# Kernel optimization log

Measured on AMD Instinct MI355X. Metric: run time of the kernel, lower is better.

Reference implementation:

```python
import jax, jax.numpy as jnp
import numpy as np

B = 131072      # batch of states
N_ACT = 40      # output_dim (Tetris action space)


def setup_inputs() -> dict:
    key = jax.random.key(0)
    ks = jax.random.split(key, 9)
    # state vector: 11 real-valued board features, 1 hold-piece id in [0,4),
    # 3 next-piece ids in [1,8) (0 is treated as invalid by the original code)
    keep = jax.random.normal(ks[0], (B, 11), dtype=jnp.float32)
    hold = jax.random.randint(ks[1], (B, 1), 0, 4).astype(jnp.float32)
    nxt = jax.random.randint(ks[2], (B, 3), 1, 8).astype(jnp.float32)
    x = jnp.concatenate([keep, hold, nxt], axis=1)  # [B, 15]
    W1 = jax.random.normal(ks[3], (36, 128), dtype=jnp.float32) * 0.1
    b1 = jnp.zeros((128,), dtype=jnp.float32)
    W2 = jax.random.normal(ks[4], (128, 512), dtype=jnp.float32) * 0.05
    b2 = jnp.zeros((512,), dtype=jnp.float32)
    W4 = jax.random.normal(ks[5], (512, N_ACT), dtype=jnp.float32) * 0.05
    b4 = jnp.zeros((N_ACT,), dtype=jnp.float32)
    return {"x": x, "W1": W1, "b1": b1, "W2": W2, "b2": b2, "W4": W4, "b4": b4}


def reference(x, W1, b1, W2, b2, W4, b4):
    B_, _ = x.shape
    keep = x[:, :11]                                      # [B, 11]
    # vectorized replacement of the per-sample .item() one-hot loop
    hold_idx = jax.lax.stop_gradient(jnp.clip(x[:, 11].astype(jnp.int32), 0, 3))
    nxt_idx = jax.lax.stop_gradient(jnp.clip(x[:, 12:15].astype(jnp.int32) - 1, 0, 6))
    hold_oh = jax.nn.one_hot(hold_idx, 4, dtype=x.dtype)  # [B, 4]
    nxt_oh = jax.nn.one_hot(nxt_idx, 7, dtype=x.dtype).reshape(B_, 21)  # [B, 21]
    inp = jnp.concatenate([keep, hold_oh, nxt_oh], axis=1)  # [B, 36]
    h = jax.nn.relu(inp @ W1 + b1)   # [B, 128]
    h = jax.nn.relu(h @ W2 + b2)     # [B, 512]
    return h @ W4 + b4               # [B, N_ACT]
```

## Files before the change

kernel.cpp:

```cpp
#include <hip/hip_runtime.h>


typedef short bf16x8 __attribute__((ext_vector_type(8)));
typedef float f32x4 __attribute__((ext_vector_type(4)));
typedef unsigned int u32;

#define NW1F 8192
#define NW2F 65536
#define NW4F 24576
#define PACK_TOTAL (NW1F + NW2F + NW4F)
#define PACK_THREADS (PACK_TOTAL / 8)

__device__ __forceinline__ unsigned short f2bf(float f) {
  union { float f; unsigned u; } a; a.f = f;
  unsigned r = a.u + 0x7fffu + ((a.u >> 16) & 1u);
  return (unsigned short)(r >> 16);
}
__device__ __forceinline__ u32 cvtpk(float lo, float hi) {
  u32 r;
  asm("v_cvt_pk_bf16_f32 %0, %1, %2" : "=v"(r) : "v"(lo), "v"(hi));
  return r;
}

__global__ void pack_weights(const float* __restrict__ W1,
                             const float* __restrict__ W2,
                             const float* __restrict__ W4,
                             unsigned short* __restrict__ wf) {
  int t = blockIdx.x * 256 + threadIdx.x;
  if (t >= PACK_THREADS) return;
  int fid = t >> 6, lane = t & 63;
  int l16 = lane & 15, quad = lane >> 4;
  float vals[8];
  if (fid < 16) {
    int mt = fid >> 1, ks = fid & 1;
    int m = mt * 16 + l16, k0 = ks * 32 + quad * 8;
#pragma unroll
    for (int j = 0; j < 8; ++j) { int k = k0 + j; vals[j] = (k < 36) ? W1[k * 128 + m] : 0.f; }
  } else if (fid < 144) {
    int f = fid - 16, mt = f >> 2, ks = f & 3;
    int m = mt * 16 + l16, k0 = ks * 32 + quad * 8;
#pragma unroll
    for (int j = 0; j < 8; ++j) vals[j] = W2[(k0 + j) * 512 + m];
  } else {
    int f = fid - 144, mt = f >> 4, ks = f & 15;
    int m = mt * 16 + l16, k0 = ks * 32 + quad * 8;
#pragma unroll
    for (int j = 0; j < 8; ++j) vals[j] = (m < 40) ? W4[(k0 + j) * 40 + m] : 0.f;
  }
  u32 p[4];
#pragma unroll
  for (int j = 0; j < 4; ++j) p[j] = cvtpk(vals[2 * j], vals[2 * j + 1]);
  *(bf16x8*)(wf + (size_t)t * 8) = *(bf16x8*)p;
}

__global__ __launch_bounds__(256, 2) void dqn_fused(
    const float* __restrict__ x,
    const unsigned short* __restrict__ wf,
    const float* __restrict__ b1,
    const float* __restrict__ b2,
    const float* __restrict__ b4,
    float* __restrict__ out) {
  __shared__ __align__(16) unsigned short sBuf[4 * 64 * 72];

  const int tid  = threadIdx.x;
  const int lane = tid & 63;
  const int wave = tid >> 6;
  const int quad = lane >> 4;
  const int l16  = lane & 15;
  const int row0 = blockIdx.x << 8;
  const int lr0  = wave * 64;
  unsigned short* su = sBuf + wave * (64 * 72);

  {
    const float* xr = x + (size_t)(row0 + lr0 + lane) * 15;
    unsigned short* dst = su + lane * 72;
    bf16x8 z = {0, 0, 0, 0, 0, 0, 0, 0};
#pragma unroll
    for (int c = 8; c < 64; c += 8) *(bf16x8*)(dst + c) = z;
    u32 p[4];
#pragma unroll
    for (int i = 0; i < 4; ++i) p[i] = cvtpk(xr[2 * i], xr[2 * i + 1]);
    *(bf16x8*)dst = *(bf16x8*)p;
    *(u32*)(dst + 8) = cvtpk(xr[8], xr[9]);
    dst[10] = f2bf(xr[10]);
    int hold = (int)xr[11]; hold = hold < 0 ? 0 : (hold > 3 ? 3 : hold);
    dst[11 + hold] = 0x3F80;
#pragma unroll
    for (int t = 0; t < 3; ++t) {
      int nx = (int)xr[12 + t] - 1; nx = nx < 0 ? 0 : (nx > 6 ? 6 : nx);
      dst[15 + t * 7 + nx] = 0x3F80;
    }
  }

  const f32x4 vzero = {0.f, 0.f, 0.f, 0.f};

  bf16x8 ib[4][2];
#pragma unroll
  for (int rg = 0; rg < 4; ++rg)
#pragma unroll
    for (int ks = 0; ks < 2; ++ks)
      ib[rg][ks] = *(const bf16x8*)(su + (rg * 16 + l16) * 72 + ks * 32 + quad * 8);

  bf16x8 af1[4][4];
#pragma unroll
  for (int half = 0; half < 2; ++half) {
    f32x4 acc1[4][4];
#pragma unroll
    for (int mtl = 0; mtl < 4; ++mtl)
#pragma unroll
      for (int rg = 0; rg < 4; ++rg) acc1[mtl][rg] = vzero;

#pragma unroll
    for (int mtl = 0; mtl < 4; ++mtl)
#pragma unroll
      for (int ks = 0; ks < 2; ++ks) {
        int mt = half * 4 + mtl;
        bf16x8 wa = *(const bf16x8*)(wf + (size_t)((mt * 2 + ks) * 64 + lane) * 8);
#pragma unroll
        for (int rg = 0; rg < 4; ++rg)
          acc1[mtl][rg] = __builtin_amdgcn_mfma_f32_16x16x32_bf16(wa, ib[rg][ks], acc1[mtl][rg], 0, 0, 0);
      }
#pragma unroll
    for (int mtl = 0; mtl < 4; ++mtl) {
      f32x4 bias = *(const f32x4*)(b1 + (half * 4 + mtl) * 16 + quad * 4);
#pragma unroll
      for (int rg = 0; rg < 4; ++rg) {
        float v0 = fmaxf(acc1[mtl][rg][0] + bias[0], 0.f);
        float v1 = fmaxf(acc1[mtl][rg][1] + bias[1], 0.f);
        float v2 = fmaxf(acc1[mtl][rg][2] + bias[2], 0.f);
        float v3 = fmaxf(acc1[mtl][rg][3] + bias[3], 0.f);
        uint2 pk = {cvtpk(v0, v1), cvtpk(v2, v3)};
        *(uint2*)(su + (rg * 16 + l16) * 72 + mtl * 16 + quad * 4) = pk;
      }
    }
#pragma unroll
    for (int rg = 0; rg < 4; ++rg)
#pragma unroll
      for (int ksl = 0; ksl < 2; ++ksl)
        af1[rg][half * 2 + ksl] =
            *(const bf16x8*)(su + (rg * 16 + l16) * 72 + ksl * 32 + quad * 8);
  }

  f32x4 accO[3][4];
#pragma unroll
  for (int mt = 0; mt < 3; ++mt)
#pragma unroll
    for (int rg = 0; rg < 4; ++rg) accO[mt][rg] = vzero;

  const unsigned short* w2f = wf + NW1F;
  const unsigned short* w4f = wf + NW1F + NW2F;

  for (int chunk = 0; chunk < 8; ++chunk) {
    __builtin_amdgcn_s_barrier();
    f32x4 acc2[4][4];
#pragma unroll
    for (int mtl = 0; mtl < 4; ++mtl)
#pragma unroll
      for (int rg = 0; rg < 4; ++rg) acc2[mtl][rg] = vzero;

#pragma unroll
    for (int ks = 0; ks < 4; ++ks)
#pragma unroll
      for (int mtl = 0; mtl < 4; ++mtl) {
        bf16x8 w = *(const bf16x8*)(w2f + (size_t)((((chunk * 4 + mtl) * 4) + ks) * 64 + lane) * 8);
#pragma unroll
        for (int rg = 0; rg < 4; ++rg)
          acc2[mtl][rg] = __builtin_amdgcn_mfma_f32_16x16x32_bf16(w, af1[rg][ks], acc2[mtl][rg], 0, 0, 0);
      }
#pragma unroll
    for (int mtl = 0; mtl < 4; ++mtl) {
      f32x4 bias = *(const f32x4*)(b2 + chunk * 64 + mtl * 16 + quad * 4);
#pragma unroll
      for (int rg = 0; rg < 4; ++rg) {
        float v0 = fmaxf(acc2[mtl][rg][0] + bias[0], 0.f);
        float v1 = fmaxf(acc2[mtl][rg][1] + bias[1], 0.f);
        float v2 = fmaxf(acc2[mtl][rg][2] + bias[2], 0.f);
        float v3 = fmaxf(acc2[mtl][rg][3] + bias[3], 0.f);
        uint2 pk = {cvtpk(v0, v1), cvtpk(v2, v3)};
        *(uint2*)(su + (rg * 16 + l16) * 72 + mtl * 16 + quad * 4) = pk;
      }
    }
#pragma unroll
    for (int ks3 = 0; ks3 < 2; ++ks3) {
      bf16x8 h[4];
#pragma unroll
      for (int rg = 0; rg < 4; ++rg)
        h[rg] = *(const bf16x8*)(su + (rg * 16 + l16) * 72 + ks3 * 32 + quad * 8);
#pragma unroll
      for (int mt3 = 0; mt3 < 3; ++mt3) {
        bf16x8 w = *(const bf16x8*)(w4f + (size_t)((mt3 * 16 + chunk * 2 + ks3) * 64 + lane) * 8);
#pragma unroll
        for (int rg = 0; rg < 4; ++rg)
          accO[mt3][rg] = __builtin_amdgcn_mfma_f32_16x16x32_bf16(w, h[rg], accO[mt3][rg], 0, 0, 0);
      }
    }
  }

#pragma unroll
  for (int mt3 = 0; mt3 < 3; ++mt3) {
    int colbase = mt3 * 16 + quad * 4;
    if (colbase < 40) {
      f32x4 bias = *(const f32x4*)(b4 + colbase);
#pragma unroll
      for (int rg = 0; rg < 4; ++rg) {
        f32x4 v = accO[mt3][rg] + bias;
        size_t row = (size_t)(row0 + lr0 + rg * 16 + l16);
        *(f32x4*)(out + row * 40 + colbase) = v;
      }
    }
  }
}

extern "C" void kernel_launch(void* const* d_in, const int* in_sizes, int n_in,
                              void* d_out, int out_size, void* d_ws, size_t ws_size,
                              hipStream_t stream) {
  const float* x  = (const float*)d_in[0];
  const float* W1 = (const float*)d_in[1];
  const float* b1 = (const float*)d_in[2];
  const float* W2 = (const float*)d_in[3];
  const float* b2 = (const float*)d_in[4];
  const float* W4 = (const float*)d_in[5];
  const float* b4 = (const float*)d_in[6];
  float* out = (float*)d_out;
  unsigned short* wf = (unsigned short*)d_ws;

  int B = in_sizes[0] / 15;

  hipLaunchKernelGGL(pack_weights, dim3((PACK_THREADS + 255) / 256), dim3(256), 0, stream,
                     W1, W2, W4, wf);
  hipLaunchKernelGGL(dqn_fused, dim3(B / 256), dim3(256), 0, stream,
                     x, wf, b1, b2, b4, out);
}
```

Baseline: 104.6 us.

## Stage W2 fragments through double-buffered LDS via global_load_lds prefetch

Layer-2 weight fragments are no longer loaded per wave straight from global memory. All four waves now cooperatively copy each 8 KB slice of W2 into a double-buffered LDS area with global_load_lds, and the next slice is prefetched while the current one is used for MFMA. The goal is to cut redundant global/L2 traffic, since every wave used to read the same W2, and to hide load latency. In exchange it adds 16 KB of LDS, which may lower occupancy, and doubles the number of block-wide barriers per chunk.

```diff
diff --git a/kernel.cpp b/kernel.cpp
--- a/kernel.cpp
+++ b/kernel.cpp
@@ -20,6 +20,11 @@
   u32 r;
   asm("v_cvt_pk_bf16_f32 %0, %1, %2" : "=v"(r) : "v"(lo), "v"(hi));
   return r;
+}
+__device__ __forceinline__ void glds16(const void* g, void* l) {
+  __builtin_amdgcn_global_load_lds(
+      (const __attribute__((address_space(1))) void*)g,
+      (__attribute__((address_space(3))) void*)l, 16, 0, 0);
 }
 
 __global__ void pack_weights(const float* __restrict__ W1,
@@ -61,6 +66,7 @@
     const float* __restrict__ b4,
     float* __restrict__ out) {
   __shared__ __align__(16) unsigned short sBuf[4 * 64 * 72];
+  __shared__ __align__(16) unsigned short sW2[2 * 4096];
 
   const int tid  = threadIdx.x;
   const int lane = tid & 63;
@@ -71,6 +77,16 @@
   const int lr0  = wave * 64;
   unsigned short* su = sBuf + wave * (64 * 72);
 
+  const unsigned short* w2f = wf + NW1F;
+  const unsigned short* w4f = wf + NW1F + NW2F;
+
+  {
+    const char* g = (const char*)w2f + wave * 2048 + lane * 16;
+    char* l = (char*)sW2 + wave * 2048;
+    glds16(g, l);
+    glds16(g + 1024, l + 1024);
+  }
+
   {
     const float* xr = x + (size_t)(row0 + lr0 + lane) * 15;
     unsigned short* dst = su + lane * 72;
@@ -147,37 +163,47 @@
 #pragma unroll
     for (int rg = 0; rg < 4; ++rg) accO[mt][rg] = vzero;
 
-  const unsigned short* w2f = wf + NW1F;
-  const unsigned short* w4f = wf + NW1F + NW2F;
-
   for (int chunk = 0; chunk < 8; ++chunk) {
-    __builtin_amdgcn_s_barrier();
-    f32x4 acc2[4][4];
-#pragma unroll
-    for (int mtl = 0; mtl < 4; ++mtl)
-#pragma unroll
-      for (int rg = 0; rg < 4; ++rg) acc2[mtl][rg] = vzero;
-
-#pragma unroll
-    for (int ks = 0; ks < 4; ++ks)
-#pragma unroll
-      for (int mtl = 0; mtl < 4; ++mtl) {
-        bf16x8 w = *(const bf16x8*)(w2f + (size_t)((((chunk * 4 + mtl) * 4) + ks) * 64 + lane) * 8);
-#pragma unroll
-        for (int rg = 0; rg < 4; ++rg)
-          acc2[mtl][rg] = __builtin_amdgcn_mfma_f32_16x16x32_bf16(w, af1[rg][ks], acc2[mtl][rg], 0, 0, 0);
-      }
-#pragma unroll
-    for (int mtl = 0; mtl < 4; ++mtl) {
-      f32x4 bias = *(const f32x4*)(b2 + chunk * 64 + mtl * 16 + quad * 4);
-#pragma unroll
-      for (int rg = 0; rg < 4; ++rg) {
-        float v0 = fmaxf(acc2[mtl][rg][0] + bias[0], 0.f);
-        float v1 = fmaxf(acc2[mtl][rg][1] + bias[1], 0.f);
-        float v2 = fmaxf(acc2[mtl][rg][2] + bias[2], 0.f);
-        float v3 = fmaxf(acc2[mtl][rg][3] + bias[3], 0.f);
-        uint2 pk = {cvtpk(v0, v1), cvtpk(v2, v3)};
-        *(uint2*)(su + (rg * 16 + l16) * 72 + mtl * 16 + quad * 4) = pk;
+#pragma unroll
+    for (int half = 0; half < 2; ++half) {
+      const int s = chunk * 2 + half;
+      __syncthreads();
+      if (s < 15) {
+        const char* g = (const char*)w2f + (size_t)(s + 1) * 8192 + wave * 2048 + lane * 16;
+        char* l = (char*)sW2 + ((s + 1) & 1) * 8192 + wave * 2048;
+        glds16(g, l);
+        glds16(g + 1024, l + 1024);
+      }
+      const unsigned short* wbuf = sW2 + (s & 1) * 4096;
+
+      f32x4 acc2[2][4];
+#pragma unroll
+      for (int ml = 0; ml < 2; ++ml)
+#pragma unroll
+        for (int rg = 0; rg < 4; ++rg) acc2[ml][rg] = vzero;
+
+#pragma unroll
+      for (int ks = 0; ks < 4; ++ks)
+#pragma unroll
+        for (int ml = 0; ml < 2; ++ml) {
+          bf16x8 w = *(const bf16x8*)(wbuf + (ml * 4 + ks) * 512 + lane * 8);
+#pragma unroll
+          for (int rg = 0; rg < 4; ++rg)
+            acc2[ml][rg] = __builtin_amdgcn_mfma_f32_16x16x32_bf16(w, af1[rg][ks], acc2[ml][rg], 0, 0, 0);
+        }
+#pragma unroll
+      for (int ml = 0; ml < 2; ++ml) {
+        int mtl = half * 2 + ml;
+        f32x4 bias = *(const f32x4*)(b2 + chunk * 64 + mtl * 16 + quad * 4);
+#pragma unroll
+        for (int rg = 0; rg < 4; ++rg) {
+          float v0 = fmaxf(acc2[ml][rg][0] + bias[0], 0.f);
+          float v1 = fmaxf(acc2[ml][rg][1] + bias[1], 0.f);
+          float v2 = fmaxf(acc2[ml][rg][2] + bias[2], 0.f);
+          float v3 = fmaxf(acc2[ml][rg][3] + bias[3], 0.f);
+          uint2 pk = {cvtpk(v0, v1), cvtpk(v2, v3)};
+          *(uint2*)(su + (rg * 16 + l16) * 72 + mtl * 16 + quad * 4) = pk;
+        }
       }
     }
 #pragma unroll
```

New measurement: 102.1 us. 1.02x faster.

## Software-prefetch weight fragments in registers and shrink blocks to two waves

Applied to the files above, without the earlier changes.

The layer-2 loop is restructured to process one 16-column tile at a time and to prefetch the next tile's W2 fragments into registers while the current MFMAs run. W4 and W1 fragments are loaded ahead of their MFMAs, and the now-unneeded per-chunk barrier is dropped since each wave only uses its own LDS slice. Blocks shrink from 256 to 128 threads with half the shared memory, doubling the grid. The aim is to hide global/L2 weight-load latency and improve scheduling flexibility, at the cost of more live registers, which could reduce occupancy.

```diff
diff --git a/kernel.cpp b/kernel.cpp
--- a/kernel.cpp
+++ b/kernel.cpp
@@ -53,23 +53,31 @@
   *(bf16x8*)(wf + (size_t)t * 8) = *(bf16x8*)p;
 }
 
-__global__ __launch_bounds__(256, 2) void dqn_fused(
+__global__ __launch_bounds__(128, 2) void dqn_fused(
     const float* __restrict__ x,
     const unsigned short* __restrict__ wf,
     const float* __restrict__ b1,
     const float* __restrict__ b2,
     const float* __restrict__ b4,
     float* __restrict__ out) {
-  __shared__ __align__(16) unsigned short sBuf[4 * 64 * 72];
+  __shared__ __align__(16) unsigned short sBuf[2 * 64 * 72];
 
   const int tid  = threadIdx.x;
   const int lane = tid & 63;
   const int wave = tid >> 6;
   const int quad = lane >> 4;
   const int l16  = lane & 15;
-  const int row0 = blockIdx.x << 8;
+  const int row0 = blockIdx.x << 7;
   const int lr0  = wave * 64;
   unsigned short* su = sBuf + wave * (64 * 72);
+
+  const unsigned short* w2f = wf + NW1F;
+  const unsigned short* w4f = wf + NW1F + NW2F;
+  const unsigned short* w2p = w2f + lane * 8;
+
+  bf16x8 curW[4];
+#pragma unroll
+  for (int k = 0; k < 4; ++k) curW[k] = *(const bf16x8*)(w2p + (size_t)k * 512);
 
   {
     const float* xr = x + (size_t)(row0 + lr0 + lane) * 15;
@@ -104,6 +112,14 @@
   bf16x8 af1[4][4];
 #pragma unroll
   for (int half = 0; half < 2; ++half) {
+    bf16x8 wa[4][2];
+#pragma unroll
+    for (int mtl = 0; mtl < 4; ++mtl)
+#pragma unroll
+      for (int ks = 0; ks < 2; ++ks)
+        wa[mtl][ks] = *(const bf16x8*)(
+            wf + (size_t)(((half * 4 + mtl) * 2 + ks) * 64 + lane) * 8);
+
     f32x4 acc1[4][4];
 #pragma unroll
     for (int mtl = 0; mtl < 4; ++mtl)
@@ -113,13 +129,11 @@
 #pragma unroll
     for (int mtl = 0; mtl < 4; ++mtl)
 #pragma unroll
-      for (int ks = 0; ks < 2; ++ks) {
-        int mt = half * 4 + mtl;
-        bf16x8 wa = *(const bf16x8*)(wf + (size_t)((mt * 2 + ks) * 64 + lane) * 8);
+      for (int ks = 0; ks < 2; ++ks)
 #pragma unroll
         for (int rg = 0; rg < 4; ++rg)
-          acc1[mtl][rg] = __builtin_amdgcn_mfma_f32_16x16x32_bf16(wa, ib[rg][ks], acc1[mtl][rg], 0, 0, 0);
-      }
+          acc1[mtl][rg] = __builtin_amdgcn_mfma_f32_16x16x32_bf16(wa[mtl][ks], ib[rg][ks], acc1[mtl][rg], 0, 0, 0);
+
 #pragma unroll
     for (int mtl = 0; mtl < 4; ++mtl) {
       f32x4 bias = *(const f32x4*)(b1 + (half * 4 + mtl) * 16 + quad * 4);
@@ -147,39 +161,47 @@
 #pragma unroll
     for (int rg = 0; rg < 4; ++rg) accO[mt][rg] = vzero;
 
-  const unsigned short* w2f = wf + NW1F;
-  const unsigned short* w4f = wf + NW1F + NW2F;
-
   for (int chunk = 0; chunk < 8; ++chunk) {
-    __builtin_amdgcn_s_barrier();
-    f32x4 acc2[4][4];
-#pragma unroll
-    for (int mtl = 0; mtl < 4; ++mtl)
-#pragma unroll
-      for (int rg = 0; rg < 4; ++rg) acc2[mtl][rg] = vzero;
-
-#pragma unroll
-    for (int ks = 0; ks < 4; ++ks)
-#pragma unroll
-      for (int mtl = 0; mtl < 4; ++mtl) {
-        bf16x8 w = *(const bf16x8*)(w2f + (size_t)((((chunk * 4 + mtl) * 4) + ks) * 64 + lane) * 8);
+    bf16x8 w4r[2][3];
+#pragma unroll
+    for (int ks3 = 0; ks3 < 2; ++ks3)
+#pragma unroll
+      for (int mt3 = 0; mt3 < 3; ++mt3)
+        w4r[ks3][mt3] = *(const bf16x8*)(
+            w4f + (size_t)((mt3 * 16 + chunk * 2 + ks3) * 64 + lane) * 8);
+
+#pragma unroll
+    for (int mtl = 0; mtl < 4; ++mtl) {
+      int fb = chunk * 16 + mtl * 4 + 4;
+      if (fb >= 128) fb = 0;
+      bf16x8 nxtW[4];
+#pragma unroll
+      for (int k = 0; k < 4; ++k)
+        nxtW[k] = *(const bf16x8*)(w2p + (size_t)(fb + k) * 512);
+
+      f32x4 acc2[4];
+#pragma unroll
+      for (int rg = 0; rg < 4; ++rg) acc2[rg] = vzero;
+#pragma unroll
+      for (int ks = 0; ks < 4; ++ks)
 #pragma unroll
         for (int rg = 0; rg < 4; ++rg)
-          acc2[mtl][rg] = __builtin_amdgcn_mfma_f32_16x16x32_bf16(w, af1[rg][ks], acc2[mtl][rg], 0, 0, 0);
-      }
-#pragma unroll
-    for (int mtl = 0; mtl < 4; ++mtl) {
+          acc2[rg] = __builtin_amdgcn_mfma_f32_16x16x32_bf16(curW[ks], af1[rg][ks], acc2[rg], 0, 0, 0);
+
       f32x4 bias = *(const f32x4*)(b2 + chunk * 64 + mtl * 16 + quad * 4);
 #pragma unroll
       for (int rg = 0; rg < 4; ++rg) {
-        float v0 = fmaxf(acc2[mtl][rg][0] + bias[0], 0.f);
-        float v1 = fmaxf(acc2[mtl][rg][1] + bias[1], 0.f);
-        float v2 = fmaxf(acc2[mtl][rg][2] + bias[2], 0.f);
-        float v3 = fmaxf(acc2[mtl][rg][3] + bias[3], 0.f);
+        float v0 = fmaxf(acc2[rg][0] + bias[0], 0.f);
+        float v1 = fmaxf(acc2[rg][1] + bias[1], 0.f);
+        float v2 = fmaxf(acc2[rg][2] + bias[2], 0.f);
+        float v3 = fmaxf(acc2[rg][3] + bias[3], 0.f);
         uint2 pk = {cvtpk(v0, v1), cvtpk(v2, v3)};
         *(uint2*)(su + (rg * 16 + l16) * 72 + mtl * 16 + quad * 4) = pk;
       }
-    }
+#pragma unroll
+      for (int k = 0; k < 4; ++k) curW[k] = nxtW[k];
+    }
+
 #pragma unroll
     for (int ks3 = 0; ks3 < 2; ++ks3) {
       bf16x8 h[4];
@@ -187,12 +209,10 @@
       for (int rg = 0; rg < 4; ++rg)
         h[rg] = *(const bf16x8*)(su + (rg * 16 + l16) * 72 + ks3 * 32 + quad * 8);
 #pragma unroll
-      for (int mt3 = 0; mt3 < 3; ++mt3) {
-        bf16x8 w = *(const bf16x8*)(w4f + (size_t)((mt3 * 16 + chunk * 2 + ks3) * 64 + lane) * 8);
+      for (int mt3 = 0; mt3 < 3; ++mt3)
 #pragma unroll
         for (int rg = 0; rg < 4; ++rg)
-          accO[mt3][rg] = __builtin_amdgcn_mfma_f32_16x16x32_bf16(w, h[rg], accO[mt3][rg], 0, 0, 0);
-      }
+          accO[mt3][rg] = __builtin_amdgcn_mfma_f32_16x16x32_bf16(w4r[ks3][mt3], h[rg], accO[mt3][rg], 0, 0, 0);
     }
   }
 
@@ -228,6 +248,6 @@
 
   hipLaunchKernelGGL(pack_weights, dim3((PACK_THREADS + 255) / 256), dim3(256), 0, stream,
                      W1, W2, W4, wf);
-  hipLaunchKernelGGL(dqn_fused, dim3(B / 256), dim3(256), 0, stream,
+  hipLaunchKernelGGL(dqn_fused, dim3(B / 128), dim3(128), 0, stream,
                      x, wf, b1, b2, b4, out);
 }
```

After: 99.53 us. 1.05x faster.
